# Performance work log

Measured on AMD Instinct MI355X. Metric: run time of the kernel, lower is better.

The kernel has to match this reference:

```python
import jax, jax.numpy as jnp
import numpy as np

B, C, H, W = 8, 21, 512, 512
MAX_M = 0.5   # args.ldam_max_m
S = 30.0      # args.ldam_s


def setup_inputs() -> dict:
    key = jax.random.key(0)
    k1, k2 = jax.random.split(key)
    pred = jax.random.normal(k1, (B, C, H, W), dtype=jnp.float32)
    target = jax.random.randint(k2, (B, H, W), 0, C, dtype=jnp.int32)  # class labels (argmax of one-hot)
    return {"pred": pred, "target": target}


def reference(pred, target):
    labels = target.reshape(-1)  # [N]
    # m_list: per-class pixel counts == sum of one-hot target over (0,2,3)
    counts = jnp.zeros((C,), dtype=pred.dtype).at[labels].add(1.0)
    m_list = 1.0 / jnp.sqrt(jnp.sqrt(counts + 1e-4))
    m_list = m_list * (MAX_M / jnp.max(m_list))

    logits = pred.transpose(0, 2, 3, 1).reshape(-1, C)  # [N, C]
    batch_m = m_list[labels]                            # gather == matmul(m_list, one_hot^T)
    onehot = jax.nn.one_hot(labels, C, dtype=logits.dtype)
    output = logits - batch_m[:, None] * onehot         # subtract margin only at target class

    logp = jax.nn.log_softmax(S * output, axis=-1)
    nll = -jnp.take_along_axis(logp, labels[:, None].astype(jnp.int32), axis=1)[:, 0]
    return jnp.mean(nll)
```

## Files before the change

### kernel.cpp

```cpp
#include <hip/hip_runtime.h>

static constexpr int   Cc  = 21;
static constexpr int   HWn = 512 * 512;
static constexpr int   Nn  = 8 * HWn;
static constexpr float MAXM  = 0.5f;
static constexpr float Sc    = 30.0f;
static constexpr float LOG2E = 1.4426950408889634f;
static constexpr float LN2   = 0.6931471805599453f;

static constexpr int HIST_BLOCKS = 512;
static constexpr int LOSS_BLOCKS = 512;

static constexpr int WS_COUNTS = 0;
static constexpr int WS_FLAG   = 96;
static constexpr int WS_SM     = 128;
static constexpr int WS_PART   = 256;

__global__ __launch_bounds__(256) void hist_kernel(const int4* __restrict__ t4,
                                                   int* __restrict__ counts) {
    __shared__ int lh[4][Cc];
    int t = threadIdx.x;
    if (t < 4 * Cc) ((int*)lh)[t] = 0;
    __syncthreads();
    int wave = t >> 6;
    int base = blockIdx.x * (256 * 4) + t;
    #pragma unroll
    for (int i = 0; i < 4; ++i) {
        int4 v = t4[base + i * 256];
        atomicAdd(&lh[wave][v.x], 1);
        atomicAdd(&lh[wave][v.y], 1);
        atomicAdd(&lh[wave][v.z], 1);
        atomicAdd(&lh[wave][v.w], 1);
    }
    __syncthreads();
    if (t < Cc)
        atomicAdd(&counts[t], lh[0][t] + lh[1][t] + lh[2][t] + lh[3][t]);
}

__global__ __launch_bounds__(64) void mlist_kernel(const int* __restrict__ counts,
                                                   float* __restrict__ sm2) {
    int t = threadIdx.x;
    float mval = 0.0f;
    if (t < Cc) {
        float cnt = (float)counts[t] + 1e-4f;
        mval = 1.0f / sqrtf(sqrtf(cnt));
    }
    float mx = mval;
    #pragma unroll
    for (int o = 32; o >= 1; o >>= 1) mx = fmaxf(mx, __shfl_down(mx, o));
    mx = __shfl(mx, 0);
    if (t < Cc) sm2[t] = Sc * LOG2E * mval * (MAXM / mx);
}

__device__ __forceinline__ void upd1(float x, int y, float smy, int c, float S2,
                                     float& m, float& s, float& v) {
    bool  isy = (c == y);
    float val = fmaf(S2, x, isy ? -smy : 0.0f);
    float mn  = fmaxf(m, val);
    s = fmaf(s, exp2f(m - mn), exp2f(val - mn));
    v = isy ? val : v;
    m = mn;
}

__global__ __launch_bounds__(256, 2) void loss_kernel(const float* __restrict__ pred,
                                                      const int* __restrict__ target,
                                                      const float* __restrict__ smg,
                                                      double* __restrict__ partial,
                                                      unsigned int* __restrict__ flag,
                                                      float* __restrict__ out) {
    __shared__ float  s_sm[Cc];
    __shared__ float  wsum[4];
    __shared__ double dsum[4];
    __shared__ bool   s_last;
    int t = threadIdx.x;
    if (t < Cc) s_sm[t] = smg[t];
    __syncthreads();

    int wave = t >> 6;
    int lane = t & 63;
    int gw   = blockIdx.x * 4 + wave;
    int P0   = gw << 10;
    int b    = P0 >> 18;
    int hw0  = P0 & (HWn - 1);
    int poff = lane * 4;
    const float* base = pred + (size_t)b * (Cc * HWn) + hw0;

    float xm[16], xs[16], xv[16], xsm[16];
    int   xy[16];
    #pragma unroll
    for (int j = 0; j < 4; ++j) {
        int4 yv = *(const int4*)&target[P0 + j * 256 + poff];
        xy[4 * j + 0] = yv.x;  xsm[4 * j + 0] = s_sm[yv.x];
        xy[4 * j + 1] = yv.y;  xsm[4 * j + 1] = s_sm[yv.y];
        xy[4 * j + 2] = yv.z;  xsm[4 * j + 2] = s_sm[yv.z];
        xy[4 * j + 3] = yv.w;  xsm[4 * j + 3] = s_sm[yv.w];
    }
    #pragma unroll
    for (int i = 0; i < 16; ++i) { xm[i] = -1e30f; xs[i] = 0.0f; xv[i] = 0.0f; }

    const float S2 = Sc * LOG2E;
    float4 bufA[4], bufB[4];

#define LOADB_(B, c) { const float* pc_ = base + (size_t)(c) * HWn + poff;      \
        B[0] = *(const float4*)(pc_);        B[1] = *(const float4*)(pc_ + 256);\
        B[2] = *(const float4*)(pc_ + 512);  B[3] = *(const float4*)(pc_ + 768); }
#define UPD4_(B, J, c)                                                              \
        upd1(B[J].x, xy[4*(J)+0], xsm[4*(J)+0], (c), S2, xm[4*(J)+0], xs[4*(J)+0], xv[4*(J)+0]); \
        upd1(B[J].y, xy[4*(J)+1], xsm[4*(J)+1], (c), S2, xm[4*(J)+1], xs[4*(J)+1], xv[4*(J)+1]); \
        upd1(B[J].z, xy[4*(J)+2], xsm[4*(J)+2], (c), S2, xm[4*(J)+2], xs[4*(J)+2], xv[4*(J)+2]); \
        upd1(B[J].w, xy[4*(J)+3], xsm[4*(J)+3], (c), S2, xm[4*(J)+3], xs[4*(J)+3], xv[4*(J)+3]);
#define PROC_(B, c) { UPD4_(B, 0, c) UPD4_(B, 1, c) UPD4_(B, 2, c) UPD4_(B, 3, c) }

    LOADB_(bufA, 0);
    #pragma unroll 1
    for (int c = 0; c < 20; c += 2) {
        LOADB_(bufB, c + 1);
        PROC_(bufA, c);
        LOADB_(bufA, c + 2);
        PROC_(bufB, c + 1);
    }
    PROC_(bufA, 20);

#undef LOADB_
#undef UPD4_
#undef PROC_

    float nll = 0.0f;
    #pragma unroll
    for (int i = 0; i < 16; ++i) nll += __log2f(xs[i]) + xm[i] - xv[i];
    nll *= LN2;

    #pragma unroll
    for (int o = 32; o >= 1; o >>= 1) nll += __shfl_down(nll, o);

    if (lane == 0) wsum[wave] = nll;
    __syncthreads();
    if (t == 0) {
        float bsum = wsum[0] + wsum[1] + wsum[2] + wsum[3];
        partial[blockIdx.x] = (double)bsum;
        __threadfence();
        unsigned done = atomicAdd(flag, 1u);
        s_last = (done == (unsigned)(LOSS_BLOCKS - 1));
    }
    __syncthreads();

    if (s_last) {
        __threadfence();
        double sm = 0.0;
        for (int i = t; i < LOSS_BLOCKS; i += 256) sm += partial[i];
        #pragma unroll
        for (int o = 32; o >= 1; o >>= 1) sm += __shfl_down(sm, o);
        if ((t & 63) == 0) dsum[t >> 6] = sm;
        __syncthreads();
        if (t == 0)
            out[0] = (float)((dsum[0] + dsum[1] + dsum[2] + dsum[3]) / (double)Nn);
    }
}

extern "C" void kernel_launch(void* const* d_in, const int* in_sizes, int n_in,
                              void* d_out, int out_size, void* d_ws, size_t ws_size,
                              hipStream_t stream) {
    const float* pred   = (const float*)d_in[0];
    const int*   target = (const int*)d_in[1];
    float*       out    = (float*)d_out;

    char* ws = (char*)d_ws;
    int*          counts  = (int*)(ws + WS_COUNTS);
    unsigned int* flag    = (unsigned int*)(ws + WS_FLAG);
    float*        sm      = (float*)(ws + WS_SM);
    double*       partial = (double*)(ws + WS_PART);

    hipMemsetAsync(d_ws, 0, 128, stream);

    hist_kernel <<<HIST_BLOCKS, 256, 0, stream>>>((const int4*)target, counts);
    mlist_kernel<<<1,           64,  0, stream>>>(counts, sm);
    loss_kernel <<<LOSS_BLOCKS, 256, 0, stream>>>(pred, target, sm,
                                                  partial, flag, out);
}
```

Baseline: 274.3 us.

## Halve pixels per wave, raise occupancy, and triple-buffer class loads

Each wave now handles 512 pixels instead of 1024, so there are twice as many loss blocks and per-thread register state is halved. Launch bounds rise to 4 blocks per SM. Loads now rotate through three buffers, prefetching two classes ahead, and the loop runs all 21 classes with clamped out-of-range loads. The goal is more memory parallelism and better latency hiding on this bandwidth-bound pass. The cost is redundant clamped loads at the tail and a larger final reduction over twice as many partials.

```diff
diff --git a/kernel.cpp b/kernel.cpp
--- a/kernel.cpp
+++ b/kernel.cpp
@@ -9,7 +9,8 @@
 static constexpr float LN2   = 0.6931471805599453f;
 
 static constexpr int HIST_BLOCKS = 512;
-static constexpr int LOSS_BLOCKS = 512;
+static constexpr int PXW         = 512;
+static constexpr int LOSS_BLOCKS = Nn / (4 * PXW);
 
 static constexpr int WS_COUNTS = 0;
 static constexpr int WS_FLAG   = 96;
@@ -52,17 +53,7 @@
     if (t < Cc) sm2[t] = Sc * LOG2E * mval * (MAXM / mx);
 }
 
-__device__ __forceinline__ void upd1(float x, int y, float smy, int c, float S2,
-                                     float& m, float& s, float& v) {
-    bool  isy = (c == y);
-    float val = fmaf(S2, x, isy ? -smy : 0.0f);
-    float mn  = fmaxf(m, val);
-    s = fmaf(s, exp2f(m - mn), exp2f(val - mn));
-    v = isy ? val : v;
-    m = mn;
-}
-
-__global__ __launch_bounds__(256, 2) void loss_kernel(const float* __restrict__ pred,
+__global__ __launch_bounds__(256, 4) void loss_kernel(const float* __restrict__ pred,
                                                       const int* __restrict__ target,
                                                       const float* __restrict__ smg,
                                                       double* __restrict__ partial,
@@ -79,55 +70,56 @@
     int wave = t >> 6;
     int lane = t & 63;
     int gw   = blockIdx.x * 4 + wave;
-    int P0   = gw << 10;
+    int P0   = gw << 9;
     int b    = P0 >> 18;
     int hw0  = P0 & (HWn - 1);
     int poff = lane * 4;
     const float* base = pred + (size_t)b * (Cc * HWn) + hw0;
 
-    float xm[16], xs[16], xv[16], xsm[16];
-    int   xy[16];
+    float xm[8], xs[8], xv[8], xsm[8];
+    int   xy[8];
     #pragma unroll
-    for (int j = 0; j < 4; ++j) {
+    for (int j = 0; j < 2; ++j) {
         int4 yv = *(const int4*)&target[P0 + j * 256 + poff];
-        xy[4 * j + 0] = yv.x;  xsm[4 * j + 0] = s_sm[yv.x];
-        xy[4 * j + 1] = yv.y;  xsm[4 * j + 1] = s_sm[yv.y];
-        xy[4 * j + 2] = yv.z;  xsm[4 * j + 2] = s_sm[yv.z];
-        xy[4 * j + 3] = yv.w;  xsm[4 * j + 3] = s_sm[yv.w];
+        xy[4 * j + 0] = yv.x;  xsm[4 * j + 0] = -s_sm[yv.x];
+        xy[4 * j + 1] = yv.y;  xsm[4 * j + 1] = -s_sm[yv.y];
+        xy[4 * j + 2] = yv.z;  xsm[4 * j + 2] = -s_sm[yv.z];
+        xy[4 * j + 3] = yv.w;  xsm[4 * j + 3] = -s_sm[yv.w];
     }
     #pragma unroll
-    for (int i = 0; i < 16; ++i) { xm[i] = -1e30f; xs[i] = 0.0f; xv[i] = 0.0f; }
+    for (int i = 0; i < 8; ++i) { xm[i] = -1e30f; xs[i] = 0.0f; xv[i] = 0.0f; }
 
     const float S2 = Sc * LOG2E;
-    float4 bufA[4], bufB[4];
+    float4 b0[2], b1[2], b2[2];
 
-#define LOADB_(B, c) { const float* pc_ = base + (size_t)(c) * HWn + poff;      \
-        B[0] = *(const float4*)(pc_);        B[1] = *(const float4*)(pc_ + 256);\
-        B[2] = *(const float4*)(pc_ + 512);  B[3] = *(const float4*)(pc_ + 768); }
-#define UPD4_(B, J, c)                                                              \
-        upd1(B[J].x, xy[4*(J)+0], xsm[4*(J)+0], (c), S2, xm[4*(J)+0], xs[4*(J)+0], xv[4*(J)+0]); \
-        upd1(B[J].y, xy[4*(J)+1], xsm[4*(J)+1], (c), S2, xm[4*(J)+1], xs[4*(J)+1], xv[4*(J)+1]); \
-        upd1(B[J].z, xy[4*(J)+2], xsm[4*(J)+2], (c), S2, xm[4*(J)+2], xs[4*(J)+2], xv[4*(J)+2]); \
-        upd1(B[J].w, xy[4*(J)+3], xsm[4*(J)+3], (c), S2, xm[4*(J)+3], xs[4*(J)+3], xv[4*(J)+3]);
-#define PROC_(B, c) { UPD4_(B, 0, c) UPD4_(B, 1, c) UPD4_(B, 2, c) UPD4_(B, 3, c) }
+#define LOADB_(B, c) { int cl_ = (c) <= 20 ? (c) : 20;                          \
+        const float* pc_ = base + (size_t)cl_ * HWn + poff;                     \
+        B[0] = *(const float4*)(pc_);  B[1] = *(const float4*)(pc_ + 256); }
+#define UPD1_(xx, I, c) { bool isy_ = ((c) == xy[I]);                           \
+        float val_ = fmaf(S2, (xx), isy_ ? xsm[I] : 0.0f);                      \
+        float mn_  = fmaxf(xm[I], val_);                                        \
+        xs[I] = fmaf(xs[I], exp2f(xm[I] - mn_), exp2f(val_ - mn_));             \
+        xv[I] = isy_ ? val_ : xv[I];  xm[I] = mn_; }
+#define PROC_(B, c) { UPD1_(B[0].x,0,c) UPD1_(B[0].y,1,c) UPD1_(B[0].z,2,c)     \
+                      UPD1_(B[0].w,3,c) UPD1_(B[1].x,4,c) UPD1_(B[1].y,5,c)     \
+                      UPD1_(B[1].z,6,c) UPD1_(B[1].w,7,c) }
 
-    LOADB_(bufA, 0);
+    LOADB_(b0, 0);
+    LOADB_(b1, 1);
     #pragma unroll 1
-    for (int c = 0; c < 20; c += 2) {
-        LOADB_(bufB, c + 1);
-        PROC_(bufA, c);
-        LOADB_(bufA, c + 2);
-        PROC_(bufB, c + 1);
+    for (int c = 0; c < 21; c += 3) {
+        LOADB_(b2, c + 2);  PROC_(b0, c);
+        LOADB_(b0, c + 3);  PROC_(b1, c + 1);
+        LOADB_(b1, c + 4);  PROC_(b2, c + 2);
     }
-    PROC_(bufA, 20);
 
 #undef LOADB_
-#undef UPD4_
+#undef UPD1_
 #undef PROC_
 
     float nll = 0.0f;
     #pragma unroll
-    for (int i = 0; i < 16; ++i) nll += __log2f(xs[i]) + xm[i] - xv[i];
+    for (int i = 0; i < 8; ++i) nll += __log2f(xs[i]) + xm[i] - xv[i];
     nll *= LN2;
 
     #pragma unroll
```

Result: slower. 299.9 us (+9.3%).
